# Kernel tuning notes

Measured on AMD Instinct MI355X. Metric: run time of the kernel, lower is better.

## Reference

```python
import jax, jax.numpy as jnp
import numpy as np

CHUNK = 128  # chunk size for the causal linear-attention recurrence
EPS = 1e-10


def _causal_numerator(q, k, v, chunk=CHUNK):
    """N_i = sum_{j<=i} (q_i . k_j) v_j, computed chunk-recurrently.

    q,k: [B,H,N,D]; v: [B,H,N,E] -> [B,H,N,E]
    """
    B, H, N, D = q.shape
    E = v.shape[-1]
    nc = N // chunk
    qc = jnp.moveaxis(q.reshape(B, H, nc, chunk, D), 2, 0)  # [nc,B,H,c,D]
    kc = jnp.moveaxis(k.reshape(B, H, nc, chunk, D), 2, 0)
    vc = jnp.moveaxis(v.reshape(B, H, nc, chunk, E), 2, 0)
    mask = jnp.tril(jnp.ones((chunk, chunk), dtype=q.dtype))  # causal within chunk

    def step(S, inp):  # S: running sum of k_j (outer) v_j -> [B,H,D,E]
        qi, ki, vi = inp
        scores = jnp.einsum('bhid,bhjd->bhij', qi, ki) * mask
        intra = jnp.einsum('bhij,bhje->bhie', scores, vi)
        inter = jnp.einsum('bhid,bhde->bhie', qi, S)
        S = S + jnp.einsum('bhjd,bhje->bhde', ki, vi)
        return S, intra + inter

    S0 = jnp.zeros((B, H, D, E), q.dtype)
    _, outs = jax.lax.scan(step, S0, (qc, kc, vc))  # [nc,B,H,c,E]
    return jnp.moveaxis(outs, 0, 2).reshape(B, H, N, E)


def _causal_denominator(q, k):
    # D_i = q_i . cumsum_j<=i k_j  -> [B,H,N]
    return jnp.einsum('bhnd,bhnd->bhn', q, jnp.cumsum(k, axis=-2))


def setup_inputs() -> dict:
    key = jax.random.key(0)
    ks = jax.random.split(key, 5)
    shape = (2, 8, 4096, 64)
    names = ['q', 'k', 'q_rot', 'k_rot', 'v']
    # feature-mapped inputs (Performer softmax features) are positive
    return {n: jax.random.uniform(ks[i], shape, dtype=jnp.float32) for i, n in enumerate(names)}


def reference(q, k, q_rot, k_rot, v):
    N = _causal_numerator(q, k, v) + _causal_numerator(q_rot, k_rot, v)
    D = _causal_denominator(q, k) + _causal_denominator(q_rot, k_rot)
    return N * (1.0 / (D + EPS))[..., None]
```

## Files before the change

kernel.cpp:

```cpp
#include <hip/hip_runtime.h>

#define SEQ 4096
#define DIM 64
#define CHUNK 128
#define NC 32
#define EPSV 1e-10f
#define KS_OFF 2097152

typedef __attribute__((ext_vector_type(8))) short s16x8;
typedef __attribute__((ext_vector_type(4))) float f32x4;

__device__ __forceinline__ unsigned short f2bf(float f) {
  unsigned int u = __float_as_uint(f);
  u += 0x7FFF + ((u >> 16) & 1);
  return (unsigned short)(u >> 16);
}
__device__ __forceinline__ s16x8 pack8(float4 a, float4 b) {
  s16x8 r;
  r[0] = (short)f2bf(a.x); r[1] = (short)f2bf(a.y); r[2] = (short)f2bf(a.z); r[3] = (short)f2bf(a.w);
  r[4] = (short)f2bf(b.x); r[5] = (short)f2bf(b.y); r[6] = (short)f2bf(b.z); r[7] = (short)f2bf(b.w);
  return r;
}

template<bool SUM>
__device__ __forceinline__ float gather_T(const float* __restrict__ gp,
                                          unsigned short* __restrict__ dst, int t) {
  int d = t & 63, w6 = t >> 6;
  float s = 0.f;
#pragma unroll
  for (int i = 0; i < 4; ++i) {
    int j8 = w6 + i * 4;
    const float* p = gp + (size_t)(j8 * 8) * DIM + d;
    float x[8];
#pragma unroll
    for (int u = 0; u < 8; ++u) x[u] = p[(size_t)u * DIM];
    if (SUM) {
#pragma unroll
      for (int u = 0; u < 8; ++u) s += x[u];
    }
    s16x8 seg;
#pragma unroll
    for (int u = 0; u < 8; ++u) seg[u] = (short)f2bf(x[u]);
    *(s16x8*)&dst[d * 136 + j8 * 8] = seg;
  }
  return s;
}

__global__ __launch_bounds__(256) void pass_a(const float* __restrict__ k0,
                                              const float* __restrict__ k1,
                                              const float* __restrict__ v,
                                              float* __restrict__ ws) {
  __shared__ __align__(16) unsigned short skT[64 * 136];
  __shared__ __align__(16) unsigned short svT[64 * 136];
  __shared__ float spart[4][64];
  int bid = blockIdx.x;
  int m = bid >> 9, rem = bid & 511, hh = rem >> 5, c = rem & 31;
  const float* kp = (m ? k1 : k0) + (size_t)hh * SEQ * DIM + (size_t)c * CHUNK * DIM;
  const float* vp = v + (size_t)hh * SEQ * DIM + (size_t)c * CHUNK * DIM;
  int t = threadIdx.x;

  float s = gather_T<true>(kp, skT, t);
  gather_T<false>(vp, svT, t);
  spart[t >> 6][t & 63] = s;
  __syncthreads();

  if (t < 64)
    ws[KS_OFF + (size_t)bid * 64 + t] = spart[0][t] + spart[1][t] + spart[2][t] + spart[3][t];

  int w = t >> 6, L = t & 63, g = L >> 4, cL = L & 15;
  f32x4 acc[4];
#pragma unroll
  for (int ct = 0; ct < 4; ++ct) acc[ct] = (f32x4){0.f, 0.f, 0.f, 0.f};
#pragma unroll
  for (int ks = 0; ks < 4; ++ks) {
    s16x8 aF = *(const s16x8*)&svT[(w * 16 + cL) * 136 + ks * 32 + g * 8];
#pragma unroll
    for (int ct = 0; ct < 4; ++ct) {
      s16x8 bF = *(const s16x8*)&skT[(ct * 16 + cL) * 136 + ks * 32 + g * 8];
      acc[ct] = __builtin_amdgcn_mfma_f32_16x16x32_bf16(aF, bF, acc[ct], 0, 0, 0);
    }
  }
  unsigned short* Sp = (unsigned short*)ws + (size_t)bid * 4096;
#pragma unroll
  for (int ct = 0; ct < 4; ++ct)
#pragma unroll
    for (int r = 0; r < 4; ++r)
      Sp[(size_t)(w * 16 + g * 4 + r) * 64 + ct * 16 + cL] = f2bf(acc[ct][r]);
}

__global__ __launch_bounds__(256) void pass_b(float* __restrict__ ws) {
  int t = threadIdx.x;
  if (blockIdx.x < 256) {
    int gid = blockIdx.x * 256 + t;
    int mh = gid >> 11, de2 = gid & 2047;
    unsigned int* p = (unsigned int*)ws + (size_t)mh * NC * 2048 + de2;
    unsigned int x[NC];
#pragma unroll
    for (int c = 0; c < NC; ++c) x[c] = p[(size_t)c * 2048];
    float r0 = 0.f, r1 = 0.f;
#pragma unroll
    for (int c = 0; c < NC; ++c) {
      unsigned int xc = x[c];
      p[(size_t)c * 2048] = (unsigned int)f2bf(r0) | ((unsigned int)f2bf(r1) << 16);
      r0 += __uint_as_float((xc & 0xFFFFu) << 16);
      r1 += __uint_as_float(xc & 0xFFFF0000u);
    }
  } else {
    int gid = (blockIdx.x - 256) * 256 + t;
    int mh = gid >> 6, d = gid & 63;
    float* p = ws + KS_OFF + (size_t)mh * NC * 64 + d;
    float x[NC];
#pragma unroll
    for (int c = 0; c < NC; ++c) x[c] = p[(size_t)c * 64];
    float run = 0.f;
#pragma unroll
    for (int c = 0; c < NC; ++c) {
      p[(size_t)c * 64] = run;
      run += x[c];
    }
  }
}

__global__ __launch_bounds__(256) void pass_c(const float* __restrict__ q0,
                                              const float* __restrict__ q1,
                                              const float* __restrict__ k0,
                                              const float* __restrict__ k1,
                                              const float* __restrict__ v,
                                              const float* __restrict__ ws,
                                              float* __restrict__ out) {
  __shared__ __align__(16) unsigned short svT[64 * 136];
  __shared__ __align__(16) unsigned short sST[64 * 72];
  __shared__ __align__(16) unsigned short sP[128 * 136];
  __shared__ float skpref[64];
  __shared__ float sden[128];

  int hh = blockIdx.x >> 5, c = blockIdx.x & 31;
  int t = threadIdx.x;
  int w = t >> 6, L = t & 63, g = L >> 4, cL = L & 15;
  size_t off = (size_t)hh * SEQ * DIM + (size_t)c * CHUNK * DIM;
  int rt0 = w, rt1 = 7 - w;

  gather_T<false>(v + off, svT, t);

  f32x4 accO[2][4];
#pragma unroll
  for (int a = 0; a < 2; ++a)
#pragma unroll
    for (int b = 0; b < 4; ++b) accO[a][b] = (f32x4){0.f, 0.f, 0.f, 0.f};
  float denfrag[2][4] = {};
  float denp[2] = {0.f, 0.f};

  const unsigned short* Sbase = (const unsigned short*)ws;

#pragma unroll
  for (int m = 0; m < 2; ++m) {
    const float* qp = (m ? q1 : q0) + off;
    const float* kp = (m ? k1 : k0) + off;
    const unsigned short* Sp = Sbase + (size_t)(m * 512 + hh * 32 + c) * 4096;
    const float* Kp = ws + KS_OFF + (size_t)(m * 512 + hh * 32 + c) * 64;

    float4 qa0[2][2], qa1[2][2];
#pragma unroll
    for (int ti = 0; ti < 2; ++ti) {
      int row = (ti ? rt1 : rt0) * 16 + cL;
#pragma unroll
      for (int h = 0; h < 2; ++h) {
        const float* qb = qp + (size_t)row * DIM + h * 32 + g * 8;
        qa0[ti][h] = *(const float4*)qb;
        qa1[ti][h] = *(const float4*)(qb + 4);
      }
    }

    if (m) __syncthreads();

#pragma unroll
    for (int p2 = 0; p2 < 2; ++p2) {
      int idx = t + p2 * 256;
      *(s16x8*)&sST[(idx >> 3) * 72 + (idx & 7) * 8] = *(const s16x8*)&Sp[idx * 8];
    }
    if (t < 64) skpref[t] = Kp[t];
    __syncthreads();

    float kpf[2][8];
#pragma unroll
    for (int h = 0; h < 2; ++h) {
      float4 c0 = *(const float4*)&skpref[h * 32 + g * 8];
      float4 c1 = *(const float4*)&skpref[h * 32 + g * 8 + 4];
      kpf[h][0] = c0.x; kpf[h][1] = c0.y; kpf[h][2] = c0.z; kpf[h][3] = c0.w;
      kpf[h][4] = c1.x; kpf[h][5] = c1.y; kpf[h][6] = c1.z; kpf[h][7] = c1.w;
    }

    s16x8 aq[2][2];
#pragma unroll
    for (int ti = 0; ti < 2; ++ti)
#pragma unroll
      for (int h = 0; h < 2; ++h) {
        float4 a0 = qa0[ti][h], a1 = qa1[ti][h];
        denp[ti] += a0.x * kpf[h][0] + a0.y * kpf[h][1] + a0.z * kpf[h][2] + a0.w * kpf[h][3]
                  + a1.x * kpf[h][4] + a1.y * kpf[h][5] + a1.z * kpf[h][6] + a1.w * kpf[h][7];
        aq[ti][h] = pack8(a0, a1);
      }

#pragma unroll
    for (int h = 0; h < 2; ++h)
#pragma unroll
      for (int et = 0; et < 4; ++et) {
        s16x8 bS = *(const s16x8*)&sST[(et * 16 + cL) * 72 + h * 32 + g * 8];
        accO[0][et] = __builtin_amdgcn_mfma_f32_16x16x32_bf16(aq[0][h], bS, accO[0][et], 0, 0, 0);
        accO[1][et] = __builtin_amdgcn_mfma_f32_16x16x32_bf16(aq[1][h], bS, accO[1][et], 0, 0, 0);
      }

    float4 kc0[2], kc1[2];
    {
      const float* kb = kp + (size_t)cL * DIM;
#pragma unroll
      for (int h = 0; h < 2; ++h) {
        kc0[h] = *(const float4*)(kb + h * 32 + g * 8);
        kc1[h] = *(const float4*)(kb + h * 32 + g * 8 + 4);
      }
    }
    for (int jt = 0; jt <= rt1; ++jt) {
      float4 kn0[2], kn1[2];
      if (jt < rt1) {
        const float* kb = kp + (size_t)((jt + 1) * 16 + cL) * DIM;
#pragma unroll
        for (int h = 0; h < 2; ++h) {
          kn0[h] = *(const float4*)(kb + h * 32 + g * 8);
          kn1[h] = *(const float4*)(kb + h * 32 + g * 8 + 4);
        }
      }
      s16x8 bK0 = pack8(kc0[0], kc1[0]);
      s16x8 bK1 = pack8(kc0[1], kc1[1]);
#pragma unroll
      for (int ti = 0; ti < 2; ++ti) {
        int rt = ti ? rt1 : rt0;
        if (jt > rt) continue;
        f32x4 C = (f32x4){0.f, 0.f, 0.f, 0.f};
        C = __builtin_amdgcn_mfma_f32_16x16x32_bf16(aq[ti][0], bK0, C, 0, 0, 0);
        C = __builtin_amdgcn_mfma_f32_16x16x32_bf16(aq[ti][1], bK1, C, 0, 0, 0);
        if (jt == rt) {
#pragma unroll
          for (int r = 0; r < 4; ++r)
            if (cL > g * 4 + r) C[r] = 0.f;
        }
#pragma unroll
        for (int r = 0; r < 4; ++r) {
          denfrag[ti][r] += C[r];
          sP[(size_t)(rt * 16 + g * 4 + r) * 136 + jt * 16 + cL] = f2bf(C[r]);
        }
      }
#pragma unroll
      for (int h = 0; h < 2; ++h) { kc0[h] = kn0[h]; kc1[h] = kn1[h]; }
    }
    {
      int rte = (rt0 & 1) ? rt1 : rt0;
#pragma unroll
      for (int r = 0; r < 4; ++r)
        sP[(size_t)(rte * 16 + g * 4 + r) * 136 + (rte + 1) * 16 + cL] = 0;
    }

    asm volatile("s_waitcnt lgkmcnt(0)" ::: "memory");

#pragma unroll
    for (int ks = 0; ks < 4; ++ks) {
      s16x8 bV[4];
#pragma unroll
      for (int et = 0; et < 4; ++et)
        bV[et] = *(const s16x8*)&svT[(et * 16 + cL) * 136 + ks * 32 + g * 8];
#pragma unroll
      for (int ti = 0; ti < 2; ++ti) {
        int rt = ti ? rt1 : rt0;
        if (ks > (rt >> 1)) continue;
        s16x8 aP = *(const s16x8*)&sP[(size_t)(rt * 16 + cL) * 136 + ks * 32 + g * 8];
#pragma unroll
        for (int et = 0; et < 4; ++et)
          accO[ti][et] = __builtin_amdgcn_mfma_f32_16x16x32_bf16(aP, bV[et], accO[ti][et], 0, 0, 0);
      }
    }
  }

#pragma unroll
  for (int ti = 0; ti < 2; ++ti) {
    denp[ti] += __shfl_xor(denp[ti], 16);
    denp[ti] += __shfl_xor(denp[ti], 32);
  }
  if (L < 16) {
    sden[rt0 * 16 + L] = denp[0];
    sden[rt1 * 16 + L] = denp[1];
  }
  __syncthreads();

  float* op = out + off;
#pragma unroll
  for (int ti = 0; ti < 2; ++ti) {
    int rt = ti ? rt1 : rt0;
#pragma unroll
    for (int r = 0; r < 4; ++r) {
      float vs = denfrag[ti][r];
      vs += __shfl_xor(vs, 1);
      vs += __shfl_xor(vs, 2);
      vs += __shfl_xor(vs, 4);
      vs += __shfl_xor(vs, 8);
      int row = rt * 16 + g * 4 + r;
      float inv = 1.f / (sden[row] + vs + EPSV);
#pragma unroll
      for (int et = 0; et < 4; ++et)
        op[(size_t)row * 64 + et * 16 + cL] = accO[ti][et][r] * inv;
    }
  }
}

extern "C" void kernel_launch(void* const* d_in, const int* in_sizes, int n_in,
                              void* d_out, int out_size, void* d_ws, size_t ws_size,
                              hipStream_t stream) {
  const float* q  = (const float*)d_in[0];
  const float* k  = (const float*)d_in[1];
  const float* qr = (const float*)d_in[2];
  const float* kr = (const float*)d_in[3];
  const float* v  = (const float*)d_in[4];
  float* out = (float*)d_out;
  float* ws  = (float*)d_ws;

  hipLaunchKernelGGL(pass_a, dim3(1024), dim3(256), 0, stream, k, kr, v, ws);
  hipLaunchKernelGGL(pass_b, dim3(264), dim3(256), 0, stream, ws);
  hipLaunchKernelGGL(pass_c, dim3(512), dim3(256), 0, stream, q, qr, k, kr, v, ws, out);
}
```

Measured before the change: 137.9 us.

## Split pass_c across 512 threads per feature map and keep P in registers

pass_c now launches 512 threads. Each pair of waves handles one row tile, with the two feature maps (q,k and q_rot,k_rot) split across the wave halves, and the partial outputs are combined through shared memory at the end. The intra-chunk score tile is computed transposed (K·Q^T) and redistributed to MFMA A-operand layout with lane shuffles, so the shared-memory sP staging buffer is gone. The denominator is accumulated directly from the masked scores. bf16 conversion now uses the hardware packed v_cvt_pk_bf16_f32 instruction. The aim is more parallelism and fewer LDS round trips, at the cost of an extra output-exchange barrier and higher register pressure under launch_bounds(512,4).

After: 139.6 us. No clear change (+1.2%).

```diff
diff --git a/kernel.cpp b/kernel.cpp
--- a/kernel.cpp
+++ b/kernel.cpp
@@ -15,33 +15,42 @@
   u += 0x7FFF + ((u >> 16) & 1);
   return (unsigned short)(u >> 16);
 }
+__device__ __forceinline__ float bf2f_lo(unsigned int x) { return __uint_as_float(x << 16); }
+
+__device__ __forceinline__ unsigned int cvtpk(float lo, float hi) {
+  unsigned int r;
+  asm("v_cvt_pk_bf16_f32 %0, %1, %2" : "=v"(r) : "v"(lo), "v"(hi));
+  return r;
+}
 __device__ __forceinline__ s16x8 pack8(float4 a, float4 b) {
-  s16x8 r;
-  r[0] = (short)f2bf(a.x); r[1] = (short)f2bf(a.y); r[2] = (short)f2bf(a.z); r[3] = (short)f2bf(a.w);
-  r[4] = (short)f2bf(b.x); r[5] = (short)f2bf(b.y); r[6] = (short)f2bf(b.z); r[7] = (short)f2bf(b.w);
-  return r;
-}
-
-template<bool SUM>
+  union { unsigned int u[4]; s16x8 v; } r;
+  r.u[0] = cvtpk(a.x, a.y); r.u[1] = cvtpk(a.z, a.w);
+  r.u[2] = cvtpk(b.x, b.y); r.u[3] = cvtpk(b.z, b.w);
+  return r.v;
+}
+
+template<bool SUM, int TPB>
 __device__ __forceinline__ float gather_T(const float* __restrict__ gp,
                                           unsigned short* __restrict__ dst, int t) {
-  int d = t & 63, w6 = t >> 6;
+  int d = t & 63, grp = t >> 6;
+  constexpr int GRPS = TPB / 64;
+  constexpr int NI = 16 / GRPS;
   float s = 0.f;
 #pragma unroll
-  for (int i = 0; i < 4; ++i) {
-    int j8 = w6 + i * 4;
+  for (int i = 0; i < NI; ++i) {
+    int j8 = grp + i * GRPS;
     const float* p = gp + (size_t)(j8 * 8) * DIM + d;
     float x[8];
 #pragma unroll
-    for (int u = 0; u < 8; ++u) x[u] = p[(size_t)u * DIM];
+    for (int u2 = 0; u2 < 8; ++u2) x[u2] = p[(size_t)u2 * DIM];
     if (SUM) {
 #pragma unroll
-      for (int u = 0; u < 8; ++u) s += x[u];
-    }
-    s16x8 seg;
-#pragma unroll
-    for (int u = 0; u < 8; ++u) seg[u] = (short)f2bf(x[u]);
-    *(s16x8*)&dst[d * 136 + j8 * 8] = seg;
+      for (int u2 = 0; u2 < 8; ++u2) s += x[u2];
+    }
+    union { unsigned int u4[4]; s16x8 v; } seg;
+#pragma unroll
+    for (int u2 = 0; u2 < 4; ++u2) seg.u4[u2] = cvtpk(x[2 * u2], x[2 * u2 + 1]);
+    *(s16x8*)&dst[d * 136 + j8 * 8] = seg.v;
   }
   return s;
 }
@@ -59,8 +68,8 @@
   const float* vp = v + (size_t)hh * SEQ * DIM + (size_t)c * CHUNK * DIM;
   int t = threadIdx.x;
 
-  float s = gather_T<true>(kp, skT, t);
-  gather_T<false>(vp, svT, t);
+  float s = gather_T<true, 256>(kp, skT, t);
+  gather_T<false, 256>(vp, svT, t);
   spart[t >> 6][t & 63] = s;
   __syncthreads();
 
@@ -102,7 +111,7 @@
     for (int c = 0; c < NC; ++c) {
       unsigned int xc = x[c];
       p[(size_t)c * 2048] = (unsigned int)f2bf(r0) | ((unsigned int)f2bf(r1) << 16);
-      r0 += __uint_as_float((xc & 0xFFFFu) << 16);
+      r0 += bf2f_lo(xc & 0xFFFFu);
       r1 += __uint_as_float(xc & 0xFFFF0000u);
     }
   } else {
@@ -121,191 +130,171 @@
   }
 }
 
-__global__ __launch_bounds__(256) void pass_c(const float* __restrict__ q0,
-                                              const float* __restrict__ q1,
-                                              const float* __restrict__ k0,
-                                              const float* __restrict__ k1,
-                                              const float* __restrict__ v,
-                                              const float* __restrict__ ws,
-                                              float* __restrict__ out) {
+__global__ __launch_bounds__(512, 4) void pass_c(const float* __restrict__ q0,
+                                                 const float* __restrict__ q1,
+                                                 const float* __restrict__ k0,
+                                                 const float* __restrict__ k1,
+                                                 const float* __restrict__ v,
+                                                 const float* __restrict__ ws,
+                                                 float* __restrict__ out) {
   __shared__ __align__(16) unsigned short svT[64 * 136];
-  __shared__ __align__(16) unsigned short sST[64 * 72];
-  __shared__ __align__(16) unsigned short sP[128 * 136];
-  __shared__ float skpref[64];
-  __shared__ float sden[128];
+  __shared__ __align__(16) union UBuf {
+    struct {
+      unsigned short sST[2][64 * 72];
+      float skpref[2][64];
+    } a;
+    float exch[128 * 66];
+  } u;
+  __shared__ float sden[2][128];
 
   int hh = blockIdx.x >> 5, c = blockIdx.x & 31;
   int t = threadIdx.x;
   int w = t >> 6, L = t & 63, g = L >> 4, cL = L & 15;
   size_t off = (size_t)hh * SEQ * DIM + (size_t)c * CHUNK * DIM;
-  int rt0 = w, rt1 = 7 - w;
-
-  gather_T<false>(v + off, svT, t);
+  const int rtS0 = w, rtS1 = 7 - w;
+
+  gather_T<false, 512>(v + off, svT, t);
+
+  {
+    int half = t >> 8, tt = t & 255;
+    const unsigned short* Sp = (const unsigned short*)ws + (size_t)(half * 512 + hh * 32 + c) * 4096;
+    const float* Kp = ws + KS_OFF + (size_t)(half * 512 + hh * 32 + c) * 64;
+#pragma unroll
+    for (int p2 = 0; p2 < 2; ++p2) {
+      int idx = tt + p2 * 256;
+      *(s16x8*)&u.a.sST[half][(idx >> 3) * 72 + (idx & 7) * 8] = *(const s16x8*)&Sp[idx * 8];
+    }
+    if (tt < 64) u.a.skpref[half][tt] = Kp[tt];
+  }
+  __syncthreads();
 
   f32x4 accO[2][4];
 #pragma unroll
   for (int a = 0; a < 2; ++a)
 #pragma unroll
     for (int b = 0; b < 4; ++b) accO[a][b] = (f32x4){0.f, 0.f, 0.f, 0.f};
-  float denfrag[2][4] = {};
-  float denp[2] = {0.f, 0.f};
-
-  const unsigned short* Sbase = (const unsigned short*)ws;
-
-#pragma unroll
-  for (int m = 0; m < 2; ++m) {
-    const float* qp = (m ? q1 : q0) + off;
-    const float* kp = (m ? k1 : k0) + off;
-    const unsigned short* Sp = Sbase + (size_t)(m * 512 + hh * 32 + c) * 4096;
-    const float* Kp = ws + KS_OFF + (size_t)(m * 512 + hh * 32 + c) * 64;
-
-    float4 qa0[2][2], qa1[2][2];
-#pragma unroll
-    for (int ti = 0; ti < 2; ++ti) {
-      int row = (ti ? rt1 : rt0) * 16 + cL;
-#pragma unroll
-      for (int h = 0; h < 2; ++h) {
-        const float* qb = qp + (size_t)row * DIM + h * 32 + g * 8;
-        qa0[ti][h] = *(const float4*)qb;
-        qa1[ti][h] = *(const float4*)(qb + 4);
+  float dent[2] = {0.f, 0.f};
+  s16x8 aq[2][2];
+
+#pragma unroll
+  for (int s2 = 0; s2 < 2; ++s2) {
+    int rt = s2 ? rtS1 : rtS0;
+    const float* qp = (s2 ? q1 : q0) + off;
+    int row = rt * 16 + cL;
+#pragma unroll
+    for (int h = 0; h < 2; ++h) {
+      const float* qb = qp + (size_t)row * DIM + h * 32 + g * 8;
+      float4 a0 = *(const float4*)qb;
+      float4 a1 = *(const float4*)(qb + 4);
+      const float* kq = &u.a.skpref[s2][h * 32 + g * 8];
+      dent[s2] += a0.x * kq[0] + a0.y * kq[1] + a0.z * kq[2] + a0.w * kq[3]
+                + a1.x * kq[4] + a1.y * kq[5] + a1.z * kq[6] + a1.w * kq[7];
+      aq[s2][h] = pack8(a0, a1);
+    }
+#pragma unroll
+    for (int h = 0; h < 2; ++h)
+#pragma unroll
+      for (int et = 0; et < 4; ++et) {
+        s16x8 bS = *(const s16x8*)&u.a.sST[s2][(et * 16 + cL) * 72 + h * 32 + g * 8];
+        accO[s2][et] = __builtin_amdgcn_mfma_f32_16x16x32_bf16(aq[s2][h], bS, accO[s2][et], 0, 0, 0);
       }
-    }
-
-    if (m) __syncthreads();
-
-#pragma unroll
-    for (int p2 = 0; p2 < 2; ++p2) {
-      int idx = t + p2 * 256;
-      *(s16x8*)&sST[(idx >> 3) * 72 + (idx & 7) * 8] = *(const s16x8*)&Sp[idx * 8];
-    }
-    if (t < 64) skpref[t] = Kp[t];
-    __syncthreads();
-
-    float kpf[2][8];
-#pragma unroll
-    for (int h = 0; h < 2; ++h) {
-      float4 c0 = *(const float4*)&skpref[h * 32 + g * 8];
-      float4 c1 = *(const float4*)&skpref[h * 32 + g * 8 + 4];
-      kpf[h][0] = c0.x; kpf[h][1] = c0.y; kpf[h][2] = c0.z; kpf[h][3] = c0.w;
-      kpf[h][4] = c1.x; kpf[h][5] = c1.y; kpf[h][6] = c1.z; kpf[h][7] = c1.w;
-    }
-
-    s16x8 aq[2][2];
-#pragma unroll
-    for (int ti = 0; ti < 2; ++ti)
-#pragma unroll
-      for (int h = 0; h < 2; ++h) {
-        float4 a0 = qa0[ti][h], a1 = qa1[ti][h];
-        denp[ti] += a0.x * kpf[h][0] + a0.y * kpf[h][1] + a0.z * kpf[h][2] + a0.w * kpf[h][3]
-                  + a1.x * kpf[h][4] + a1.y * kpf[h][5] + a1.z * kpf[h][6] + a1.w * kpf[h][7];
-        aq[ti][h] = pack8(a0, a1);
-      }
-
-#pragma unroll
-    for (int h = 0; h < 2; ++h)
-#pragma unroll
-      for (int et = 0; et < 4; ++et) {
-        s16x8 bS = *(const s16x8*)&sST[(et * 16 + cL) * 72 + h * 32 + g * 8];
-        accO[0][et] = __builtin_amdgcn_mfma_f32_16x16x32_bf16(aq[0][h], bS, accO[0][et], 0, 0, 0);
-        accO[1][et] = __builtin_amdgcn_mfma_f32_16x16x32_bf16(aq[1][h], bS, accO[1][et], 0, 0, 0);
-      }
-
-    float4 kc0[2], kc1[2];
-    {
-      const float* kb = kp + (size_t)cL * DIM;
-#pragma unroll
-      for (int h = 0; h < 2; ++h) {
-        kc0[h] = *(const float4*)(kb + h * 32 + g * 8);
-        kc1[h] = *(const float4*)(kb + h * 32 + g * 8 + 4);
-      }
-    }
-    for (int jt = 0; jt <= rt1; ++jt) {
-      float4 kn0[2], kn1[2];
-      if (jt < rt1) {
-        const float* kb = kp + (size_t)((jt + 1) * 16 + cL) * DIM;
-#pragma unroll
-        for (int h = 0; h < 2; ++h) {
-          kn0[h] = *(const float4*)(kb + h * 32 + g * 8);
-          kn1[h] = *(const float4*)(kb + h * 32 + g * 8 + 4);
+  }
+
+  {
+    int srcA = cL + ((g & 1) << 5), srcB = srcA + 16;
+    bool hiG = g >= 2;
+#pragma unroll
+    for (int s2 = 0; s2 < 2; ++s2) {
+      int rt = s2 ? rtS1 : rtS0;
+      const float* kp = (s2 ? k1 : k0) + off;
+      for (int ks = 0; ks <= (rt >> 1); ++ks) {
+        unsigned int E0e, E1e;
+        {
+          int jt = 2 * ks;
+          const float* kb = kp + (size_t)(jt * 16 + cL) * DIM;
+          float4 b0 = *(const float4*)(kb + g * 8);
+          float4 b1 = *(const float4*)(kb + g * 8 + 4);
+          float4 b2 = *(const float4*)(kb + 32 + g * 8);
+          float4 b3 = *(const float4*)(kb + 32 + g * 8 + 4);
+          s16x8 kf0 = pack8(b0, b1), kf1 = pack8(b2, b3);
+          f32x4 C = (f32x4){0.f, 0.f, 0.f, 0.f};
+          C = __builtin_amdgcn_mfma_f32_16x16x32_bf16(kf0, aq[s2][0], C, 0, 0, 0);
+          C = __builtin_amdgcn_mfma_f32_16x16x32_bf16(kf1, aq[s2][1], C, 0, 0, 0);
+          if (jt == rt) {
+#pragma unroll
+            for (int r = 0; r < 4; ++r)
+              if (g * 4 + r > cL) C[r] = 0.f;
+          }
+          dent[s2] += C[0] + C[1] + C[2] + C[3];
+          E0e = cvtpk(C[0], C[1]); E1e = cvtpk(C[2], C[3]);
+        }
+        int S0o = 0, S1o = 0, S2o = 0, S3o = 0;
+        if (2 * ks + 1 <= rt) {
+          int jt = 2 * ks + 1;
+          const float* kb = kp + (size_t)(jt * 16 + cL) * DIM;
+          float4 b0 = *(const float4*)(kb + g * 8);
+          float4 b1 = *(const float4*)(kb + g * 8 + 4);
+          float4 b2 = *(const float4*)(kb + 32 + g * 8);
+          float4 b3 = *(const float4*)(kb + 32 + g * 8 + 4);
+          s16x8 kf0 = pack8(b0, b1), kf1 = pack8(b2, b3);
+          f32x4 C = (f32x4){0.f, 0.f, 0.f, 0.f};
+          C = __builtin_amdgcn_mfma_f32_16x16x32_bf16(kf0, aq[s2][0], C, 0, 0, 0);
+          C = __builtin_amdgcn_mfma_f32_16x16x32_bf16(kf1, aq[s2][1], C, 0, 0, 0);
+          if (jt == rt) {
+#pragma unroll
+            for (int r = 0; r < 4; ++r)
+              if (g * 4 + r > cL) C[r] = 0.f;
+          }
+          dent[s2] += C[0] + C[1] + C[2] + C[3];
+          unsigned int E0o = cvtpk(C[0], C[1]), E1o = cvtpk(C[2], C[3]);
+          S0o = __shfl((int)E0o, srcA); S1o = __shfl((int)E1o, srcA);
+          S2o = __shfl((int)E0o, srcB); S3o = __shfl((int)E1o, srcB);
+        }
+        int S0e = __shfl((int)E0e, srcA); int S1e = __shfl((int)E1e, srcA);
+        int S2e = __shfl((int)E0e, srcB); int S3e = __shfl((int)E1e, srcB);
+        union { int d4[4]; s16x8 v8; } ap;
+        ap.d4[0] = hiG ? S0o : S0e;
+        ap.d4[1] = hiG ? S1o : S1e;
+        ap.d4[2] = hiG ? S2o : S2e;
+        ap.d4[3] = hiG ? S3o : S3e;
+#pragma unroll
+        for (int et = 0; et < 4; ++et) {
+          s16x8 bV = *(const s16x8*)&svT[(et * 16 + cL) * 136 + ks * 32 + g * 8];
+          accO[s2][et] = __builtin_amdgcn_mfma_f32_16x16x32_bf16(ap.v8, bV, accO[s2][et], 0, 0, 0);
         }
       }
-      s16x8 bK0 = pack8(kc0[0], kc1[0]);
-      s16x8 bK1 = pack8(kc0[1], kc1[1]);
-#pragma unroll
-      for (int ti = 0; ti < 2; ++ti) {
-        int rt = ti ? rt1 : rt0;
-        if (jt > rt) continue;
-        f32x4 C = (f32x4){0.f, 0.f, 0.f, 0.f};
-        C = __builtin_amdgcn_mfma_f32_16x16x32_bf16(aq[ti][0], bK0, C, 0, 0, 0);
-        C = __builtin_amdgcn_mfma_f32_16x16x32_bf16(aq[ti][1], bK1, C, 0, 0, 0);
-        if (jt == rt) {
-#pragma unroll
-          for (int r = 0; r < 4; ++r)
-            if (cL > g * 4 + r) C[r] = 0.f;
-        }
-#pragma unroll
-        for (int r = 0; r < 4; ++r) {
-          denfrag[ti][r] += C[r];
-          sP[(size_t)(rt * 16 + g * 4 + r) * 136 + jt * 16 + cL] = f2bf(C[r]);
-        }
-      }
-#pragma unroll
-      for (int h = 0; h < 2; ++h) { kc0[h] = kn0[h]; kc1[h] = kn1[h]; }
-    }
-    {
-      int rte = (rt0 & 1) ? rt1 : rt0;
-#pragma unroll
-      for (int r = 0; r < 4; ++r)
-        sP[(size_t)(rte * 16 + g * 4 + r) * 136 + (rte + 1) * 16 + cL] = 0;
-    }
-
-    asm volatile("s_waitcnt lgkmcnt(0)" ::: "memory");
-
-#pragma unroll
-    for (int ks = 0; ks < 4; ++ks) {
-      s16x8 bV[4];
-#pragma unroll
-      for (int et = 0; et < 4; ++et)
-        bV[et] = *(const s16x8*)&svT[(et * 16 + cL) * 136 + ks * 32 + g * 8];
-#pragma unroll
-      for (int ti = 0; ti < 2; ++ti) {
-        int rt = ti ? rt1 : rt0;
-        if (ks > (rt >> 1)) continue;
-        s16x8 aP = *(const s16x8*)&sP[(size_t)(rt * 16 + cL) * 136 + ks * 32 + g * 8];
-#pragma unroll
-        for (int et = 0; et < 4; ++et)
-          accO[ti][et] = __builtin_amdgcn_mfma_f32_16x16x32_bf16(aP, bV[et], accO[ti][et], 0, 0, 0);
-      }
-    }
-  }
-
-#pragma unroll
-  for (int ti = 0; ti < 2; ++ti) {
-    denp[ti] += __shfl_xor(denp[ti], 16);
-    denp[ti] += __shfl_xor(denp[ti], 32);
+    }
+  }
+
+#pragma unroll
+  for (int s2 = 0; s2 < 2; ++s2) {
+    float dt = dent[s2];
+    dt += __shfl_xor(dt, 16);
+    dt += __shfl_xor(dt, 32);
+    dent[s2] = dt;
   }
   if (L < 16) {
-    sden[rt0 * 16 + L] = denp[0];
-    sden[rt1 * 16 + L] = denp[1];
+    sden[0][rtS0 * 16 + L] = dent[0];
+    sden[1][rtS1 * 16 + L] = dent[1];
   }
   __syncthreads();
 
+#pragma unroll
+  for (int et = 0; et < 4; ++et)
+#pragma unroll
+    for (int r = 0; r < 4; ++r)
+      u.exch[(rtS1 * 16 + g * 4 + r) * 66 + et * 16 + cL] = accO[1][et][r];
+  __syncthreads();
+
   float* op = out + off;
 #pragma unroll
-  for (int ti = 0; ti < 2; ++ti) {
-    int rt = ti ? rt1 : rt0;
-#pragma unroll
-    for (int r = 0; r < 4; ++r) {
-      float vs = denfrag[ti][r];
-      vs += __shfl_xor(vs, 1);
-      vs += __shfl_xor(vs, 2);
-      vs += __shfl_xor(vs, 4);
-      vs += __shfl_xor(vs, 8);
-      int row = rt * 16 + g * 4 + r;
-      float inv = 1.f / (sden[row] + vs + EPSV);
-#pragma unroll
-      for (int et = 0; et < 4; ++et)
-        op[(size_t)row * 64 + et * 16 + cL] = accO[ti][et][r] * inv;
+  for (int r = 0; r < 4; ++r) {
+    int row = rtS0 * 16 + g * 4 + r;
+    float inv = 1.f / (sden[0][row] + sden[1][row] + EPSV);
+#pragma unroll
+    for (int et = 0; et < 4; ++et) {
+      float O = accO[0][et][r] + u.exch[row * 66 + et * 16 + cL];
+      op[(size_t)row * DIM + et * 16 + cL] = O * inv;
     }
   }
 }
@@ -323,5 +312,5 @@
 
   hipLaunchKernelGGL(pass_a, dim3(1024), dim3(256), 0, stream, k, kr, v, ws);
   hipLaunchKernelGGL(pass_b, dim3(264), dim3(256), 0, stream, ws);
-  hipLaunchKernelGGL(pass_c, dim3(512), dim3(256), 0, stream, q, qr, k, kr, v, ws, out);
-}
+  hipLaunchKernelGGL(pass_c, dim3(512), dim3(512), 0, stream, q, qr, k, kr, v, ws, out);
+}
```
